# Kernel optimization log

Hardware: AMD Instinct MI355X
Metric: run time of the kernel (lower is better)

Reference implementation:

```python
import jax, jax.numpy as jnp
import numpy as np

NBINS = 256

def setup_inputs() -> dict:
    key = jax.random.key(0)
    inputs = jax.random.uniform(key, (32, 512, 512, 3), dtype=jnp.float32)
    return {"inputs": inputs}

def reference(inputs) -> jnp.ndarray:
    # inputs: [B, H, W, C] with values assumed in [0, 1]
    B, H, W, C = inputs.shape
    n = H * W
    # tf.histogram_fixed_width bin index: clip(floor(nbins*(v-min)/(max-min)), 0, nbins-1)
    idx = jnp.clip(jnp.floor(inputs * NBINS).astype(jnp.int32), 0, NBINS - 1)  # [B,H,W,C]
    # Combined segment id per (batch, channel, bin) -> single fused scatter-add
    bc = jnp.arange(B)[:, None, None] * C + jnp.arange(C)[None, None, :]      # [B,1,C]
    seg = (bc * NBINS + idx.reshape(B, n, C)).reshape(-1)                      # [B*n*C]
    hist = jax.ops.segment_sum(
        jnp.ones((B * n * C,), dtype=jnp.float32), seg, num_segments=B * C * NBINS
    ).reshape(B, C, NBINS)
    # per-channel normalization: each channel histogram sums to H*W
    hist = hist / jnp.float32(n)
    # output [B, nbins, C] to match tf.stack(histograms, axis=-1)
    return jnp.transpose(hist, (0, 2, 1))
```

## Files before the change

### kernel.cpp

```cpp
#include <hip/hip_runtime.h>

#define NBINS 256
#define NCH 3
#define NWAVES 4
#define BLOCK 256
#define ELEMS_PER_THREAD 12

__global__ __launch_bounds__(BLOCK) void hist_kernel(const float* __restrict__ in,
                                                     unsigned int* __restrict__ counts,
                                                     int blocksPerBatch,
                                                     int floatsPerBatch) {
    __shared__ unsigned int h[NWAVES][NCH * NBINS];

    const int tid = threadIdx.x;
    for (int i = tid; i < NWAVES * NCH * NBINS; i += BLOCK) {
        ((unsigned int*)h)[i] = 0u;
    }
    __syncthreads();

    const int b     = blockIdx.x / blocksPerBatch;
    const int chunk = blockIdx.x % blocksPerBatch;
    const int chunkFloats = floatsPerBatch / blocksPerBatch;
    const float* base = in + (size_t)b * floatsPerBatch + (size_t)chunk * chunkFloats;
    const int w = tid >> 6;

    const int floatsPerIter = BLOCK * ELEMS_PER_THREAD;
    const int iters = chunkFloats / floatsPerIter;

    for (int it = 0; it < iters; ++it) {
        const float4* p = (const float4*)(base + (size_t)it * floatsPerIter
                                               + (size_t)tid * ELEMS_PER_THREAD);
        float4 v0 = p[0];
        float4 v1 = p[1];
        float4 v2 = p[2];
        float v[ELEMS_PER_THREAD] = {v0.x, v0.y, v0.z, v0.w,
                                     v1.x, v1.y, v1.z, v1.w,
                                     v2.x, v2.y, v2.z, v2.w};
#pragma unroll
        for (int j = 0; j < ELEMS_PER_THREAD; ++j) {
            int bin = (int)floorf(v[j] * 256.0f);
            bin = bin < 0 ? 0 : (bin > NBINS - 1 ? NBINS - 1 : bin);
            const int c = j % NCH;
            atomicAdd(&h[w][c * NBINS + bin], 1u);
        }
    }
    __syncthreads();

    unsigned int* dst = counts + (size_t)b * (NCH * NBINS);
    for (int i = tid; i < NCH * NBINS; i += BLOCK) {
        unsigned int s = h[0][i] + h[1][i] + h[2][i] + h[3][i];
        if (s) atomicAdd(&dst[i], s);
    }
}

__global__ __launch_bounds__(BLOCK) void finalize_kernel(const unsigned int* __restrict__ counts,
                                                         float* __restrict__ out,
                                                         int n, float inv_n) {
    int i = blockIdx.x * BLOCK + threadIdx.x;
    if (i >= n) return;
    int c   = i % NCH;
    int bin = (i / NCH) % NBINS;
    int b   = i / (NCH * NBINS);
    out[i] = (float)counts[(size_t)b * (NCH * NBINS) + c * NBINS + bin] * inv_n;
}

extern "C" void kernel_launch(void* const* d_in, const int* in_sizes, int n_in,
                              void* d_out, int out_size, void* d_ws, size_t ws_size,
                              hipStream_t stream) {
    const float* in = (const float*)d_in[0];
    float* out = (float*)d_out;

    const int floatsPerBatch = 512 * 512 * 3;
    const int total = in_sizes[0];
    const int B = total / floatsPerBatch;
    const int n = 512 * 512;

    unsigned int* counts = (unsigned int*)d_ws;
    hipMemsetAsync(d_ws, 0, (size_t)B * NCH * NBINS * sizeof(unsigned int), stream);

    const int blocksPerBatch = 32;
    hist_kernel<<<B * blocksPerBatch, BLOCK, 0, stream>>>(in, counts, blocksPerBatch,
                                                          floatsPerBatch);

    const int outN = B * NBINS * NCH;
    finalize_kernel<<<(outN + BLOCK - 1) / BLOCK, BLOCK, 0, stream>>>(
        counts, out, outN, 1.0f / (float)n);
}
```

Baseline: 28.16 us.

## Fuse normalization into histogram kernel and double block size

Drops the separate finalize kernel: each block now scales its partial counts by 1/n and float-atomically adds them straight into the transposed output, which is zeroed by a memset. The block size goes from 256 to 512 threads with 8 per-wave shared histograms, so each block covers twice as much data per iteration. This saves a kernel launch and the intermediate count buffer. In exchange it relies on float atomics, so summation order is nondeterministic, but the partial sums are small integer multiples of a power of two and should add exactly. Each block also now uses twice the shared memory.

```diff
diff --git a/kernel.cpp b/kernel.cpp
--- a/kernel.cpp
+++ b/kernel.cpp
@@ -2,14 +2,15 @@
 
 #define NBINS 256
 #define NCH 3
-#define NWAVES 4
-#define BLOCK 256
+#define BLOCK 512
+#define NWAVES 8
 #define ELEMS_PER_THREAD 12
 
-__global__ __launch_bounds__(BLOCK) void hist_kernel(const float* __restrict__ in,
-                                                     unsigned int* __restrict__ counts,
-                                                     int blocksPerBatch,
-                                                     int floatsPerBatch) {
+__global__ __launch_bounds__(BLOCK, 8) void hist_kernel(const float* __restrict__ in,
+                                                        float* __restrict__ out,
+                                                        int blocksPerBatch,
+                                                        int floatsPerBatch,
+                                                        float inv_n) {
     __shared__ unsigned int h[NWAVES][NCH * NBINS];
 
     const int tid = threadIdx.x;
@@ -46,22 +47,17 @@
     }
     __syncthreads();
 
-    unsigned int* dst = counts + (size_t)b * (NCH * NBINS);
+    float* dst = out + (size_t)b * (NCH * NBINS);
     for (int i = tid; i < NCH * NBINS; i += BLOCK) {
-        unsigned int s = h[0][i] + h[1][i] + h[2][i] + h[3][i];
-        if (s) atomicAdd(&dst[i], s);
+        unsigned int s = 0;
+#pragma unroll
+        for (int wv = 0; wv < NWAVES; ++wv) s += h[wv][i];
+        if (s) {
+            const int c   = i >> 8;
+            const int bin = i & (NBINS - 1);
+            atomicAdd(&dst[bin * NCH + c], (float)s * inv_n);
+        }
     }
-}
-
-__global__ __launch_bounds__(BLOCK) void finalize_kernel(const unsigned int* __restrict__ counts,
-                                                         float* __restrict__ out,
-                                                         int n, float inv_n) {
-    int i = blockIdx.x * BLOCK + threadIdx.x;
-    if (i >= n) return;
-    int c   = i % NCH;
-    int bin = (i / NCH) % NBINS;
-    int b   = i / (NCH * NBINS);
-    out[i] = (float)counts[(size_t)b * (NCH * NBINS) + c * NBINS + bin] * inv_n;
 }
 
 extern "C" void kernel_launch(void* const* d_in, const int* in_sizes, int n_in,
@@ -73,16 +69,11 @@
     const int floatsPerBatch = 512 * 512 * 3;
     const int total = in_sizes[0];
     const int B = total / floatsPerBatch;
-    const int n = 512 * 512;
+    const float inv_n = 1.0f / (float)(512 * 512);
 
-    unsigned int* counts = (unsigned int*)d_ws;
-    hipMemsetAsync(d_ws, 0, (size_t)B * NCH * NBINS * sizeof(unsigned int), stream);
+    hipMemsetAsync(d_out, 0, (size_t)out_size * sizeof(float), stream);
 
     const int blocksPerBatch = 32;
-    hist_kernel<<<B * blocksPerBatch, BLOCK, 0, stream>>>(in, counts, blocksPerBatch,
-                                                          floatsPerBatch);
-
-    const int outN = B * NBINS * NCH;
-    finalize_kernel<<<(outN + BLOCK - 1) / BLOCK, BLOCK, 0, stream>>>(
-        counts, out, outN, 1.0f / (float)n);
+    hist_kernel<<<B * blocksPerBatch, BLOCK, 0, stream>>>(in, out, blocksPerBatch,
+                                                          floatsPerBatch, inv_n);
 }
```

After: 29.34 us. 4.2% more time.
